# Optimization experiments

Hardware: AMD Instinct MI355X
Metric: run time of the kernel (lower is better)

The kernel has to match this reference:

```python
import jax, jax.numpy as jnp
import numpy as np

B, N, C, G, H, DK = 8, 128, 128, 2, 4, 32
BN_SCALE = float(1.0 / np.sqrt(1.0 + 1e-5))  # eval-mode BatchNorm with running_mean=0, var=1, gamma=1, beta=0


def _l1norm(x):
    # F.normalize(p=1, dim=-1)
    return x / jnp.maximum(jnp.sum(jnp.abs(x), -1, keepdims=True), 1e-12)


def _bn(x):
    return x * BN_SCALE


def _lrelu(x):
    return jax.nn.leaky_relu(x, 0.01)


def setup_inputs() -> dict:
    key = jax.random.key(0)
    ks = jax.random.split(key, 14)
    p = lambda i, shape: jax.random.normal(ks[i], shape, jnp.float32) * 0.05
    return {
        "vp": jax.random.normal(ks[0], (B, N, C), jnp.float32),
        "ep0": jax.random.uniform(ks[1], (B, N, N), jnp.float32),
        # PointSimilarity_Pre 1x1-conv stack (stored as [in, out] matrices)
        "ps_pre_w1": p(2, (C, 2 * C)), "ps_pre_w2": p(3, (2 * C, C)),
        "ps_pre_w3": p(4, (C, 1)), "ps_pre_b3": jnp.zeros((1,), jnp.float32),
        # Per-generation PointSimilarity2 stacks
        "ps_w1": p(5, (G, C, 2 * C)), "ps_w2": p(6, (G, 2 * C, C)),
        "ps_w3": p(7, (G, C, 1)), "ps_b3": jnp.zeros((G, 1), jnp.float32),
        # Per-generation D2PAgg stacks (input is cat(vp, aggr) -> 2C channels)
        "d2p_w1": p(8, (G, 2 * C, 2 * C)), "d2p_w2": p(9, (G, 2 * C, C)),
        # Per-generation multi-head attention projections (d_model=C, n_head*d_k=C)
        "mha_wq": p(10, (G, C, H * DK)), "mha_wk": p(11, (G, C, H * DK)),
    }


def _psim(vp, ep_last, w1, w2, w3, b3, kval):
    # pairwise l2 distance features: [B, N, N, C]
    sim = (vp[:, :, None, :] - vp[:, None, :, :]) ** 2
    h = _lrelu(_bn(jnp.einsum('bijc,co->bijo', sim, w1)))
    h = _lrelu(_bn(jnp.einsum('bijc,co->bijo', h, w2)))
    e = jax.nn.sigmoid(jnp.einsum('bijc,co->bijo', h, w3)[..., 0] + b3)
    eye = jnp.eye(vp.shape[1], dtype=vp.dtype)
    ep_last = ep_last * (1.0 - eye)
    ep_sum = jnp.sum(ep_last, -1, keepdims=True)
    e = e * ep_last
    if kval is not None:  # neighbor attention via top-k sparsification
        _, idx = jax.lax.top_k(e, kval)
        b_i = jnp.arange(e.shape[0])[:, None, None]
        r_i = jnp.arange(e.shape[1])[None, :, None]
        mask = jnp.zeros_like(e).at[b_i, r_i, idx].set(1.0)
        e = e * mask
    e = _l1norm(e) * ep_sum
    e = e + eye + 1e-6
    e = e / jnp.sum(e, 2, keepdims=True)
    return e


def _d2p(ep, vp, w1, w2):
    eye = jnp.eye(vp.shape[1], dtype=vp.dtype)
    edge = _l1norm(ep * (1.0 - eye))
    aggr = jnp.einsum('bij,bjc->bic', edge, vp)  # bmm aggregation
    nf = jnp.concatenate([vp, aggr], -1)         # [B, N, 2C]
    h = _lrelu(_bn(nf @ w1))
    return _lrelu(_bn(h @ w2))


def _mha(vp, wq, wk):
    b, n, _ = vp.shape
    q = (vp @ wq).reshape(b, n, H, DK)
    k = (vp @ wk).reshape(b, n, H, DK)
    attn = jax.nn.softmax(jnp.einsum('bqhd,bkhd->bhqk', q, k) / np.sqrt(DK), axis=-1)
    return attn.mean(1)  # average heads -> [B, N, N]


def reference(vp, ep0, ps_pre_w1, ps_pre_w2, ps_pre_w3, ps_pre_b3,
              ps_w1, ps_w2, ps_w3, ps_b3, d2p_w1, d2p_w2, mha_wq, mha_wk):
    ep = _psim(vp, ep0, ps_pre_w1, ps_pre_w2, ps_pre_w3, ps_pre_b3, None)
    for g in range(G):
        attn = _mha(vp, mha_wq[g], mha_wk[g])
        vp = _d2p(ep * attn, vp, d2p_w1[g], d2p_w2[g])
        kval = int(N * (1.0 - 0.1 * (g + 1)))
        ep = _psim(vp, ep, ps_w1[g], ps_w2[g], ps_w3[g], ps_b3[g], kval)
    return ep
```

## Files before the change

### kernel.cpp

```cpp
#include <hip/hip_runtime.h>

typedef __bf16 bf16x8 __attribute__((ext_vector_type(8)));
typedef float floatx4 __attribute__((ext_vector_type(4)));

#define MFMA(a, b, c) __builtin_amdgcn_mfma_f32_16x16x32_bf16(a, b, c, 0, 0, 0)

#define BNS 0.9999950000374997f
#define LRELU(x) ((x) > 0.f ? (x) : 0.01f * (x))

__device__ inline float wave_sum(float v) {
#pragma unroll
  for (int s = 32; s > 0; s >>= 1) v += __shfl_xor(v, s, 64);
  return v;
}
__device__ inline float wave_max(float v) {
#pragma unroll
  for (int s = 32; s > 0; s >>= 1) v = fmaxf(v, __shfl_xor(v, s, 64));
  return v;
}

__global__ __launch_bounds__(256) void k_prep(const float* __restrict__ pre_w1,
                                              const float* __restrict__ ps_w1,
                                              const float* __restrict__ pre_w2,
                                              const float* __restrict__ ps_w2,
                                              const float* __restrict__ dw1,
                                              const float* __restrict__ dw2,
                                              const float* __restrict__ mwq,
                                              const float* __restrict__ mwk,
                                              __bf16* __restrict__ w1b,
                                              __bf16* __restrict__ w2b,
                                              __bf16* __restrict__ d1i,
                                              __bf16* __restrict__ d2i,
                                              __bf16* __restrict__ qki) {
  const int tt = blockIdx.x * 256 + threadIdx.x;
  bf16x8 v;
  if (tt < 24576) {
    const int buf = tt / 12288;
    const int r = tt % 12288;
    const int set = r >> 12;
    const int q = r & 4095;
    const int ln = q & 63, qd = ln >> 4, cc = ln & 15;
    const int wv = (q >> 6) & 3;
    if (buf == 0) {
      const int kt = (q >> 8) & 3, qtr = (q >> 10) & 3;
      const float* src = (set == 0) ? pre_w1 : ps_w1 + (size_t)(set - 1) * 32768;
      const float* p = src + (size_t)(kt * 32 + qd * 8) * 256 + qtr * 64 + wv * 16 + cc;
#pragma unroll
      for (int jj = 0; jj < 8; jj++) v[jj] = (__bf16)p[jj * 256];
      *(bf16x8*)&w1b[(size_t)set * 32768 + q * 8] = v;
    } else {
      const int kt = (q >> 8) & 1, nt = (q >> 9) & 1, qtr = (q >> 10) & 3;
      const float* src = (set == 0) ? pre_w2 : ps_w2 + (size_t)(set - 1) * 32768;
      const float* p = src + (size_t)(qtr * 64 + kt * 32 + qd * 8) * 128 + wv * 32 + nt * 16 + cc;
#pragma unroll
      for (int jj = 0; jj < 8; jj++) v[jj] = (__bf16)p[jj * 128];
      *(bf16x8*)&w2b[(size_t)set * 32768 + q * 8] = v;
    }
  } else if (tt < 40960) {
    const int u = tt - 24576;
    const int gen = u >> 13, r = u & 8191;
    const int nt = r >> 9, kt = (r >> 6) & 7, ln = r & 63;
    const int qd = ln >> 4, cc = ln & 15;
    const float* src = dw1 + (size_t)gen * 65536 + (size_t)(kt * 32 + qd * 8) * 256 + nt * 16 + cc;
#pragma unroll
    for (int jj = 0; jj < 8; jj++) v[jj] = (__bf16)src[jj * 256];
    *(bf16x8*)&d1i[((size_t)gen * 65536) + (size_t)r * 8] = v;
  } else if (tt < 49152) {
    const int u = tt - 40960;
    const int gen = u >> 12, r = u & 4095;
    const int nt = r >> 9, kt = (r >> 6) & 7, ln = r & 63;
    const int qd = ln >> 4, cc = ln & 15;
    const float* src = dw2 + (size_t)gen * 32768 + (size_t)(kt * 32 + qd * 8) * 128 + nt * 16 + cc;
#pragma unroll
    for (int jj = 0; jj < 8; jj++) v[jj] = (__bf16)src[jj * 128];
    *(bf16x8*)&d2i[((size_t)gen * 32768) + (size_t)r * 8] = v;
  } else if (tt < 57344) {
    const int u = tt - 49152;
    const int gen = u >> 12, r = u & 4095, qk = r >> 11, r2 = r & 2047;
    const int cb = r2 >> 7, o = r2 & 127;
    const float* src = (qk ? mwk : mwq) + (size_t)gen * 16384 + (size_t)(cb * 8) * 128 + o;
#pragma unroll
    for (int jj = 0; jj < 8; jj++) v[jj] = (__bf16)src[jj * 128];
    *(bf16x8*)&qki[(size_t)((((gen * 2 + qk) * 16 + cb) * 128 + o)) * 8] = v;
  }
}

__global__ void __launch_bounds__(256, 3)
k_psim(const float* __restrict__ vp, const float* __restrict__ ep_in,
       float* __restrict__ ep_out,
       const __bf16* __restrict__ w1b, const __bf16* __restrict__ w2b,
       const float* __restrict__ w3, const float* __restrict__ b3,
       int kval, float* __restrict__ outp) {
  __shared__ __bf16 simf[16384];
  __shared__ __bf16 hbf[8192];
  __shared__ float ep_row[128];
  __shared__ float e_row[128];
  __shared__ float w3s[128];
  __shared__ float red[256];
  __shared__ float red2[4];

  const int tid = threadIdx.x;
  const int b = blockIdx.x >> 7, i = blockIdx.x & 127;
  const float* vpb = vp + ((size_t)b << 14);
  const float* vpi = vpb + (i << 7);
  const size_t rowoff = ((size_t)blockIdx.x) << 7;

  const int wv = tid >> 6;
  const int ln = tid & 63;
  const int qd = ln >> 4;
  const int cc = ln & 15;

  {
    const int j = tid >> 1;
    const int c0 = (tid & 1) << 6;
    const int m = j >> 4, ccr = j & 15;
    const float* vpj = vpb + (j << 7) + c0;
    const float* vpx = vpi + c0;
#pragma unroll
    for (int c = 0; c < 64; c += 8) {
      const int gc = c0 + c;
      const int kt = gc >> 5, qdw = (gc >> 3) & 3;
      float4 a0 = *(const float4*)(vpj + c);
      float4 a1 = *(const float4*)(vpj + c + 4);
      float4 b0 = *(const float4*)(vpx + c);
      float4 b1 = *(const float4*)(vpx + c + 4);
      bf16x8 t;
      float d;
      d = a0.x - b0.x; t[0] = (__bf16)(d * d);
      d = a0.y - b0.y; t[1] = (__bf16)(d * d);
      d = a0.z - b0.z; t[2] = (__bf16)(d * d);
      d = a0.w - b0.w; t[3] = (__bf16)(d * d);
      d = a1.x - b1.x; t[4] = (__bf16)(d * d);
      d = a1.y - b1.y; t[5] = (__bf16)(d * d);
      d = a1.z - b1.z; t[6] = (__bf16)(d * d);
      d = a1.w - b1.w; t[7] = (__bf16)(d * d);
      *(bf16x8*)&simf[(((kt << 3) + m) << 6 | (qdw << 4 | ccr)) << 3] = t;
    }
    if (tid < 128) {
      ep_row[tid] = (tid == i) ? 0.f : ep_in[rowoff + tid];
      w3s[tid] = w3[tid];
    }
  }

  bf16x8 bw[4], bw2[2][2];
#pragma unroll
  for (int kt = 0; kt < 4; kt++)
    bw[kt] = *(const bf16x8*)&w1b[(((0 * 4 + kt) * 4 + wv) * 64 + ln) * 8];
#pragma unroll
  for (int nt = 0; nt < 2; nt++)
#pragma unroll
    for (int kt = 0; kt < 2; kt++)
      bw2[nt][kt] = *(const bf16x8*)&w2b[((((0 * 2 + nt) * 2 + kt) * 4 + wv) * 64 + ln) * 8];

  __syncthreads();

  floatx4 acc2[8][2];
#pragma unroll
  for (int m = 0; m < 8; m++) {
    acc2[m][0] = (floatx4){0.f, 0.f, 0.f, 0.f};
    acc2[m][1] = (floatx4){0.f, 0.f, 0.f, 0.f};
  }

  const int h1h = wv >> 1;
  const int h1qd = ((wv & 1) << 1) | (cc >> 3);
  const int h1jj = cc & 7;

#pragma unroll
  for (int qtr = 0; qtr < 4; qtr++) {
    bf16x8 bwn[4], bw2n[2][2];
    if (qtr < 3) {
#pragma unroll
      for (int kt = 0; kt < 4; kt++)
        bwn[kt] = *(const bf16x8*)&w1b[((((qtr + 1) * 4 + kt) * 4 + wv) * 64 + ln) * 8];
#pragma unroll
      for (int nt = 0; nt < 2; nt++)
#pragma unroll
        for (int kt = 0; kt < 2; kt++)
          bw2n[nt][kt] = *(const bf16x8*)&w2b[(((((qtr + 1) * 2 + nt) * 2 + kt) * 4 + wv) * 64 + ln) * 8];
    }

#pragma unroll
    for (int m2 = 0; m2 < 8; m2 += 2) {
      bf16x8 af0[4], af1[4];
#pragma unroll
      for (int kt = 0; kt < 4; kt++) {
        af0[kt] = *(const bf16x8*)&simf[(((kt << 3) + m2) << 6 | ln) << 3];
        af1[kt] = *(const bf16x8*)&simf[(((kt << 3) + m2 + 1) << 6 | ln) << 3];
      }
      floatx4 x0 = (floatx4){0.f, 0.f, 0.f, 0.f};
      floatx4 x1 = (floatx4){0.f, 0.f, 0.f, 0.f};
#pragma unroll
      for (int kt = 0; kt < 4; kt++) {
        x0 = MFMA(af0[kt], bw[kt], x0);
        x1 = MFMA(af1[kt], bw[kt], x1);
      }
#pragma unroll
      for (int r = 0; r < 4; r++) {
        float v0 = x0[r] * BNS;
        float v1 = x1[r] * BNS;
        hbf[(((h1h * 8 + m2) * 64) + h1qd * 16 + qd * 4 + r) * 8 + h1jj] = (__bf16)LRELU(v0);
        hbf[(((h1h * 8 + m2 + 1) * 64) + h1qd * 16 + qd * 4 + r) * 8 + h1jj] = (__bf16)LRELU(v1);
      }
    }
    __syncthreads();

#pragma unroll
    for (int m = 0; m < 8; m++) {
      bf16x8 a0 = *(const bf16x8*)&hbf[((m << 6) | ln) << 3];
      bf16x8 a1 = *(const bf16x8*)&hbf[(((8 + m) << 6) | ln) << 3];
      acc2[m][0] = MFMA(a0, bw2[0][0], acc2[m][0]);
      acc2[m][1] = MFMA(a0, bw2[1][0], acc2[m][1]);
      acc2[m][0] = MFMA(a1, bw2[0][1], acc2[m][0]);
      acc2[m][1] = MFMA(a1, bw2[1][1], acc2[m][1]);
    }
    __syncthreads();

    if (qtr < 3) {
#pragma unroll
      for (int kt = 0; kt < 4; kt++) bw[kt] = bwn[kt];
#pragma unroll
      for (int nt = 0; nt < 2; nt++)
#pragma unroll
        for (int kt = 0; kt < 2; kt++) bw2[nt][kt] = bw2n[nt][kt];
    }
  }

  {
    const int seg = wv;
#pragma unroll
    for (int m = 0; m < 8; m++)
#pragma unroll
      for (int nt = 0; nt < 2; nt++) {
        const int q2 = (nt << 1) | (cc >> 3);
#pragma unroll
        for (int r = 0; r < 4; r++) {
          float v = acc2[m][nt][r] * BNS;
          simf[(((seg * 8 + m) * 64) + q2 * 16 + qd * 4 + r) * 8 + (cc & 7)] = (__bf16)LRELU(v);
        }
      }
  }
  __syncthreads();

  {
    const int j = tid & 127, hh = tid >> 7;
    const int m = j >> 4, R = j & 15;
    float s = 0.f;
#pragma unroll
    for (int sg = 0; sg < 2; sg++) {
      const int seg = hh * 2 + sg;
#pragma unroll
      for (int q3 = 0; q3 < 4; q3++) {
        bf16x8 f = *(const bf16x8*)&simf[(((seg * 8 + m) * 64) + q3 * 16 + R) * 8];
        const float* wp = &w3s[seg * 32 + q3 * 8];
#pragma unroll
        for (int jj = 0; jj < 8; jj++) s += (float)f[jj] * wp[jj];
      }
    }
    red[tid] = s;
  }
  __syncthreads();
  if (tid < 128) {
    float s = red[tid] + red[tid + 128] + b3[0];
    float sg = 1.f / (1.f + expf(-s));
    e_row[tid] = sg * ep_row[tid];
  }
  __syncthreads();

  {
    float v = (tid < 128) ? ep_row[tid] : 0.f;
    float w = wave_sum(v);
    if (ln == 0) red2[wv] = w;
  }
  __syncthreads();
  const float ep_sum = red2[0] + red2[1];

  if (kval > 0) {
    const int j = tid & 127, hh = tid >> 7;
    const float v = e_row[j];
    int cnt = 0;
    const int base = hh << 6;
#pragma unroll 8
    for (int jj = 0; jj < 64; jj++) {
      float u = e_row[base + jj];
      cnt += (u > v || (u == v && (base + jj) < j)) ? 1 : 0;
    }
    red[tid] = (float)cnt;
  }
  __syncthreads();

  float em = 0.f;
  if (tid < 128) {
    float v = e_row[tid];
    if (kval > 0) {
      int cnt = (int)red[tid] + (int)red[tid + 128];
      em = (cnt < kval) ? v : 0.f;
    } else {
      em = v;
    }
  }
  {
    float w = wave_sum((tid < 128) ? em : 0.f);
    if (ln == 0) red2[wv] = w;
  }
  __syncthreads();
  const float l1 = red2[0] + red2[1];
  __syncthreads();

  const float scale = ep_sum / fmaxf(l1, 1e-12f);
  float val = 0.f;
  if (tid < 128) val = em * scale + ((tid == i) ? 1.f : 0.f) + 1e-6f;
  {
    float w = wave_sum((tid < 128) ? val : 0.f);
    if (ln == 0) red2[wv] = w;
  }
  __syncthreads();
  const float rsum = red2[0] + red2[1];

  if (tid < 128) {
    float o = val / rsum;
    ep_out[rowoff + tid] = o;
    if (outp) outp[rowoff + tid] = o;
  }
}

__global__ __launch_bounds__(256) void k_qk(const float* __restrict__ vp,
                                            const __bf16* __restrict__ qkw,
                                            float* __restrict__ qo,
                                            float* __restrict__ ko) {
  __shared__ float vr[128];
  const int t = threadIdx.x;
  const size_t rowoff = ((size_t)blockIdx.x) << 7;
  if (t < 128) vr[t] = vp[rowoff + t];
  __syncthreads();
  const int o = t & 127;
  const __bf16* base = qkw + ((t >> 7) ? 16384 : 0);
  const float4* vr4 = (const float4*)vr;
  float a = 0.f;
#pragma unroll
  for (int cb = 0; cb < 16; cb++) {
    bf16x8 w8 = *(const bf16x8*)&base[(cb * 128 + o) * 8];
    float4 v0 = vr4[2 * cb], v1 = vr4[2 * cb + 1];
    a += v0.x * (float)w8[0] + v0.y * (float)w8[1] + v0.z * (float)w8[2] + v0.w * (float)w8[3] +
         v1.x * (float)w8[4] + v1.y * (float)w8[5] + v1.z * (float)w8[6] + v1.w * (float)w8[7];
  }
  float* dst = (t < 128) ? qo : ko;
  dst[rowoff + o] = a;
}

__global__ __launch_bounds__(256) void k_attn_agg(const float* __restrict__ qv,
                                                  const float* __restrict__ kv,
                                                  const float* __restrict__ ep,
                                                  const float* __restrict__ vp_in,
                                                  float* __restrict__ agg) {
  __shared__ float qi[256];
  __shared__ float sbuf[1024];
  __shared__ float er[256];
  __shared__ float pbuf[2048];
  __shared__ float red2[4];

  const int tid = threadIdx.x;
  const int wv = tid >> 6, ln = tid & 63;
  const int b = blockIdx.x >> 6;
  const int r0 = (blockIdx.x & 63) * 2;
  const size_t rowoff0 = ((size_t)(b * 128 + r0)) << 7;
  const float* vpbb = vp_in + ((size_t)b << 14);

  qi[tid] = qv[rowoff0 + tid];
  __syncthreads();

  {
    const int j = tid & 127, hh = tid >> 7;
    const float* krow = kv + (((size_t)(b * 128 + j)) << 7);
    const int h0 = hh * 2, h1 = hh * 2 + 1;
    float s00 = 0.f, s01 = 0.f, s10 = 0.f, s11 = 0.f;
#pragma unroll
    for (int d = 0; d < 32; d += 4) {
      float4 k0 = *(const float4*)(krow + h0 * 32 + d);
      float4 k1 = *(const float4*)(krow + h1 * 32 + d);
      s00 += qi[h0 * 32 + d] * k0.x + qi[h0 * 32 + d + 1] * k0.y +
             qi[h0 * 32 + d + 2] * k0.z + qi[h0 * 32 + d + 3] * k0.w;
      s01 += qi[h1 * 32 + d] * k1.x + qi[h1 * 32 + d + 1] * k1.y +
             qi[h1 * 32 + d + 2] * k1.z + qi[h1 * 32 + d + 3] * k1.w;
      s10 += qi[128 + h0 * 32 + d] * k0.x + qi[128 + h0 * 32 + d + 1] * k0.y +
             qi[128 + h0 * 32 + d + 2] * k0.z + qi[128 + h0 * 32 + d + 3] * k0.w;
      s11 += qi[128 + h1 * 32 + d] * k1.x + qi[128 + h1 * 32 + d + 1] * k1.y +
             qi[128 + h1 * 32 + d + 2] * k1.z + qi[128 + h1 * 32 + d + 3] * k1.w;
    }
    const float sc = 0.17677669529663687f;
    sbuf[(0 * 4 + h0) * 128 + j] = s00 * sc;
    sbuf[(0 * 4 + h1) * 128 + j] = s01 * sc;
    sbuf[(1 * 4 + h0) * 128 + j] = s10 * sc;
    sbuf[(1 * 4 + h1) * 128 + j] = s11 * sc;
  }
  __syncthreads();

  {
    const int g = wv;
#pragma unroll
    for (int row = 0; row < 2; row++) {
      float a = sbuf[(row * 4 + g) * 128 + ln];
      float bb = sbuf[(row * 4 + g) * 128 + 64 + ln];
      float mx = wave_max(fmaxf(a, bb));
      float e0 = expf(a - mx), e1 = expf(bb - mx);
      float Z = wave_sum(e0 + e1);
      sbuf[(row * 4 + g) * 128 + ln] = e0 / Z;
      sbuf[(row * 4 + g) * 128 + 64 + ln] = e1 / Z;
    }
  }
  __syncthreads();

  {
    const int row = tid >> 7, j = tid & 127;
    float attn = 0.25f * (sbuf[(row * 4) * 128 + j] + sbuf[(row * 4 + 1) * 128 + j] +
                          sbuf[(row * 4 + 2) * 128 + j] + sbuf[(row * 4 + 3) * 128 + j]);
    float eraw = (j == r0 + row) ? 0.f : ep[rowoff0 + tid] * attn;
    float w = wave_sum(eraw);
    if (ln == 0) red2[wv] = w;
    __syncthreads();
    float l1row = red2[row * 2] + red2[row * 2 + 1];
    er[tid] = eraw / fmaxf(l1row, 1e-12f);
  }
  __syncthreads();

  {
    const int cg = tid & 31, jg = tid >> 5;
    float4 a0 = {0.f, 0.f, 0.f, 0.f}, a1 = {0.f, 0.f, 0.f, 0.f};
#pragma unroll
    for (int jj = 0; jj < 16; jj++) {
      const int j = jg * 16 + jj;
      float4 v = *(const float4*)(vpbb + (j << 7) + (cg << 2));
      float e0 = er[j], e1 = er[128 + j];
      a0.x += e0 * v.x; a0.y += e0 * v.y; a0.z += e0 * v.z; a0.w += e0 * v.w;
      a1.x += e1 * v.x; a1.y += e1 * v.y; a1.z += e1 * v.z; a1.w += e1 * v.w;
    }
    *(float4*)&pbuf[(jg * 32 + cg) * 4] = a0;
    *(float4*)&pbuf[1024 + (jg * 32 + cg) * 4] = a1;
  }
  __syncthreads();
  {
    const int row = tid >> 7, c = tid & 127;
    float s = 0.f;
#pragma unroll
    for (int jg = 0; jg < 8; jg++) s += pbuf[(row << 10) + jg * 128 + c];
    agg[rowoff0 + tid] = s;
  }
}

__global__ __launch_bounds__(256) void k_mlp(const float* __restrict__ vp_in,
                                             const float* __restrict__ agg,
                                             const __bf16* __restrict__ d1,
                                             const __bf16* __restrict__ d2,
                                             float* __restrict__ vp_out) {
  __shared__ __bf16 hls[4096];
  const int tid = threadIdx.x;
  const int wv = tid >> 6, ln = tid & 63, qd = ln >> 4, cc = ln & 15;
  const int row = (blockIdx.x << 4) + cc;

  bf16x8 af[8];
#pragma unroll
  for (int kt = 0; kt < 4; kt++) {
    const float* p = vp_in + (size_t)row * 128 + kt * 32 + qd * 8;
    float4 v0 = *(const float4*)p, v1 = *(const float4*)(p + 4);
    bf16x8 t;
    t[0] = (__bf16)v0.x; t[1] = (__bf16)v0.y; t[2] = (__bf16)v0.z; t[3] = (__bf16)v0.w;
    t[4] = (__bf16)v1.x; t[5] = (__bf16)v1.y; t[6] = (__bf16)v1.z; t[7] = (__bf16)v1.w;
    af[kt] = t;
  }
#pragma unroll
  for (int kt = 0; kt < 4; kt++) {
    const float* p = agg + (size_t)row * 128 + kt * 32 + qd * 8;
    float4 v0 = *(const float4*)p, v1 = *(const float4*)(p + 4);
    bf16x8 t;
    t[0] = (__bf16)v0.x; t[1] = (__bf16)v0.y; t[2] = (__bf16)v0.z; t[3] = (__bf16)v0.w;
    t[4] = (__bf16)v1.x; t[5] = (__bf16)v1.y; t[6] = (__bf16)v1.z; t[7] = (__bf16)v1.w;
    af[4 + kt] = t;
  }

#pragma unroll
  for (int nt = 0; nt < 4; nt++) {
    const int ntg = wv * 4 + nt;
    floatx4 acc = (floatx4){0.f, 0.f, 0.f, 0.f};
#pragma unroll
    for (int kt = 0; kt < 8; kt++) {
      bf16x8 bw = *(const bf16x8*)&d1[((size_t)(ntg * 8 + kt) * 64 + ln) * 8];
      acc = MFMA(af[kt], bw, acc);
    }
    const int col = ntg * 16 + cc;
    const int kt2 = col >> 5, qd2 = (col >> 3) & 3, jjs = col & 7;
#pragma unroll
    for (int r = 0; r < 4; r++) {
      float h = acc[r] * BNS;
      const int m = qd * 4 + r;
      hls[((kt2 * 64) + qd2 * 16 + m) * 8 + jjs] = (__bf16)LRELU(h);
    }
  }
  __syncthreads();

  bf16x8 a2[8];
#pragma unroll
  for (int kt2 = 0; kt2 < 8; kt2++)
    a2[kt2] = *(const bf16x8*)&hls[(kt2 * 64 + ln) * 8];
#pragma unroll
  for (int nt = 0; nt < 2; nt++) {
    const int ntg = wv * 2 + nt;
    floatx4 o = (floatx4){0.f, 0.f, 0.f, 0.f};
#pragma unroll
    for (int kt2 = 0; kt2 < 8; kt2++) {
      bf16x8 bw = *(const bf16x8*)&d2[((size_t)(ntg * 8 + kt2) * 64 + ln) * 8];
      o = MFMA(a2[kt2], bw, o);
    }
    const int col = ntg * 16 + cc;
#pragma unroll
    for (int r = 0; r < 4; r++) {
      float v = o[r] * BNS;
      const int m = qd * 4 + r;
      vp_out[(size_t)((blockIdx.x << 4) + m) * 128 + col] = LRELU(v);
    }
  }
}

extern "C" void kernel_launch(void* const* d_in, const int* in_sizes, int n_in,
                              void* d_out, int out_size, void* d_ws, size_t ws_size,
                              hipStream_t stream) {
  const float* vp0    = (const float*)d_in[0];
  const float* ep0    = (const float*)d_in[1];
  const float* pre_w1 = (const float*)d_in[2];
  const float* pre_w2 = (const float*)d_in[3];
  const float* pre_w3 = (const float*)d_in[4];
  const float* pre_b3 = (const float*)d_in[5];
  const float* ps_w1  = (const float*)d_in[6];
  const float* ps_w2  = (const float*)d_in[7];
  const float* ps_w3  = (const float*)d_in[8];
  const float* ps_b3  = (const float*)d_in[9];
  const float* dw1    = (const float*)d_in[10];
  const float* dw2    = (const float*)d_in[11];
  const float* mwq    = (const float*)d_in[12];
  const float* mwk    = (const float*)d_in[13];

  char* ws = (char*)d_ws;
  float* ep   = (float*)(ws);
  float* vpb  = (float*)(ws + (512ull << 10));
  float* vpa  = (float*)(ws + (1024ull << 10));
  float* qf   = (float*)(ws + (1536ull << 10));
  float* kf   = (float*)(ws + (2048ull << 10));
  __bf16* w1b = (__bf16*)(ws + (2560ull << 10));
  __bf16* w2b = (__bf16*)(ws + (2560ull << 10) + 196608);
  __bf16* d1i = (__bf16*)(ws + (2560ull << 10) + 393216);
  __bf16* d2i = (__bf16*)(ws + (2560ull << 10) + 655360);
  __bf16* qki = (__bf16*)(ws + (2560ull << 10) + 786432);
  float* agg  = (float*)(ws + (2560ull << 10) + 917504);
  float* outp = (float*)d_out;

  k_prep<<<224, 256, 0, stream>>>(pre_w1, ps_w1, pre_w2, ps_w2, dw1, dw2, mwq, mwk,
                                  w1b, w2b, d1i, d2i, qki);

  k_psim<<<1024, 256, 0, stream>>>(vp0, ep0, ep, w1b, w2b, pre_w3, pre_b3, 0, nullptr);

  k_qk<<<1024, 256, 0, stream>>>(vp0, qki, qf, kf);
  k_attn_agg<<<512, 256, 0, stream>>>(qf, kf, ep, vp0, agg);
  k_mlp<<<64, 256, 0, stream>>>(vp0, agg, d1i, d2i, vpb);
  k_psim<<<1024, 256, 0, stream>>>(vpb, ep, ep, w1b + 32768, w2b + 32768,
                                   ps_w3, ps_b3, 115, nullptr);

  k_qk<<<1024, 256, 0, stream>>>(vpb, qki + 32768, qf, kf);
  k_attn_agg<<<512, 256, 0, stream>>>(qf, kf, ep, vpb, agg);
  k_mlp<<<64, 256, 0, stream>>>(vpb, agg, d1i + 65536, d2i + 32768, vpa);
  k_psim<<<1024, 256, 0, stream>>>(vpa, ep, ep, w1b + 65536, w2b + 65536,
                                   ps_w3 + 128, ps_b3 + 1, 102, outp);
}
```

Before: 222.4 us.

## Shrink psim LDS footprint and register pressure to fit four blocks per CU

Raises the psim kernel's occupancy target from 3 to 4 blocks per CU. It halves the hidden-layer LDS buffer by splitting each quarter's row tiles into two halves with an extra barrier pair, and aliases the small scratch arrays onto that buffer. It also drops the prefetch of next-quarter weights and keeps the ep row in a register to reduce VGPR pressure. The trade is more synchronisation and exposed global weight-load latency in exchange for more resident waves to hide latency.

```diff
diff --git a/kernel.cpp b/kernel.cpp
--- a/kernel.cpp
+++ b/kernel.cpp
@@ -85,19 +85,19 @@
   }
 }
 
-__global__ void __launch_bounds__(256, 3)
+__global__ void __launch_bounds__(256, 4)
 k_psim(const float* __restrict__ vp, const float* __restrict__ ep_in,
        float* __restrict__ ep_out,
        const __bf16* __restrict__ w1b, const __bf16* __restrict__ w2b,
        const float* __restrict__ w3, const float* __restrict__ b3,
        int kval, float* __restrict__ outp) {
   __shared__ __bf16 simf[16384];
-  __shared__ __bf16 hbf[8192];
-  __shared__ float ep_row[128];
-  __shared__ float e_row[128];
-  __shared__ float w3s[128];
-  __shared__ float red[256];
-  __shared__ float red2[4];
+  __shared__ __align__(16) char sc2[8192];
+  __bf16* hbf   = (__bf16*)sc2;
+  float* red    = (float*)sc2;
+  float* e_row  = (float*)(sc2 + 1024);
+  float* red2   = (float*)(sc2 + 1536);
+  float* w3s    = (float*)(sc2 + 1552);
 
   const int tid = threadIdx.x;
   const int b = blockIdx.x >> 7, i = blockIdx.x & 127;
@@ -110,6 +110,7 @@
   const int qd = ln >> 4;
   const int cc = ln & 15;
 
+  float ep_reg = 0.f;
   {
     const int j = tid >> 1;
     const int c0 = (tid & 1) << 6;
@@ -136,22 +137,8 @@
       d = a1.w - b1.w; t[7] = (__bf16)(d * d);
       *(bf16x8*)&simf[(((kt << 3) + m) << 6 | (qdw << 4 | ccr)) << 3] = t;
     }
-    if (tid < 128) {
-      ep_row[tid] = (tid == i) ? 0.f : ep_in[rowoff + tid];
-      w3s[tid] = w3[tid];
-    }
-  }
-
-  bf16x8 bw[4], bw2[2][2];
-#pragma unroll
-  for (int kt = 0; kt < 4; kt++)
-    bw[kt] = *(const bf16x8*)&w1b[(((0 * 4 + kt) * 4 + wv) * 64 + ln) * 8];
-#pragma unroll
-  for (int nt = 0; nt < 2; nt++)
-#pragma unroll
-    for (int kt = 0; kt < 2; kt++)
-      bw2[nt][kt] = *(const bf16x8*)&w2b[((((0 * 2 + nt) * 2 + kt) * 4 + wv) * 64 + ln) * 8];
-
+    if (tid < 128) ep_reg = (tid == i) ? 0.f : ep_in[rowoff + tid];
+  }
   __syncthreads();
 
   floatx4 acc2[8][2];
@@ -165,63 +152,55 @@
   const int h1qd = ((wv & 1) << 1) | (cc >> 3);
   const int h1jj = cc & 7;
 
-#pragma unroll
   for (int qtr = 0; qtr < 4; qtr++) {
-    bf16x8 bwn[4], bw2n[2][2];
-    if (qtr < 3) {
-#pragma unroll
-      for (int kt = 0; kt < 4; kt++)
-        bwn[kt] = *(const bf16x8*)&w1b[((((qtr + 1) * 4 + kt) * 4 + wv) * 64 + ln) * 8];
-#pragma unroll
-      for (int nt = 0; nt < 2; nt++)
-#pragma unroll
-        for (int kt = 0; kt < 2; kt++)
-          bw2n[nt][kt] = *(const bf16x8*)&w2b[(((((qtr + 1) * 2 + nt) * 2 + kt) * 4 + wv) * 64 + ln) * 8];
-    }
-
-#pragma unroll
-    for (int m2 = 0; m2 < 8; m2 += 2) {
-      bf16x8 af0[4], af1[4];
-#pragma unroll
-      for (int kt = 0; kt < 4; kt++) {
-        af0[kt] = *(const bf16x8*)&simf[(((kt << 3) + m2) << 6 | ln) << 3];
-        af1[kt] = *(const bf16x8*)&simf[(((kt << 3) + m2 + 1) << 6 | ln) << 3];
+    bf16x8 bw[4], bw2[2][2];
+#pragma unroll
+    for (int kt = 0; kt < 4; kt++)
+      bw[kt] = *(const bf16x8*)&w1b[((((qtr * 4 + kt) * 4 + wv) * 64) + ln) * 8];
+#pragma unroll
+    for (int nt = 0; nt < 2; nt++)
+#pragma unroll
+      for (int kt = 0; kt < 2; kt++)
+        bw2[nt][kt] = *(const bf16x8*)&w2b[(((((qtr * 2 + nt) * 2 + kt) * 4 + wv) * 64) + ln) * 8];
+
+    for (int mh = 0; mh < 2; mh++) {
+#pragma unroll
+      for (int m2p = 0; m2p < 4; m2p += 2) {
+        const int m2 = 4 * mh + m2p;
+        bf16x8 af0[4], af1[4];
+#pragma unroll
+        for (int kt = 0; kt < 4; kt++) {
+          af0[kt] = *(const bf16x8*)&simf[(((kt << 3) + m2) << 6 | ln) << 3];
+          af1[kt] = *(const bf16x8*)&simf[(((kt << 3) + m2 + 1) << 6 | ln) << 3];
+        }
+        floatx4 x0 = (floatx4){0.f, 0.f, 0.f, 0.f};
+        floatx4 x1 = (floatx4){0.f, 0.f, 0.f, 0.f};
+#pragma unroll
+        for (int kt = 0; kt < 4; kt++) {
+          x0 = MFMA(af0[kt], bw[kt], x0);
+          x1 = MFMA(af1[kt], bw[kt], x1);
+        }
+#pragma unroll
+        for (int r = 0; r < 4; r++) {
+          float v0 = x0[r] * BNS;
+          float v1 = x1[r] * BNS;
+          hbf[(((h1h * 4 + m2p) * 64) + h1qd * 16 + qd * 4 + r) * 8 + h1jj] = (__bf16)LRELU(v0);
+          hbf[(((h1h * 4 + m2p + 1) * 64) + h1qd * 16 + qd * 4 + r) * 8 + h1jj] = (__bf16)LRELU(v1);
+        }
       }
-      floatx4 x0 = (floatx4){0.f, 0.f, 0.f, 0.f};
-      floatx4 x1 = (floatx4){0.f, 0.f, 0.f, 0.f};
-#pragma unroll
-      for (int kt = 0; kt < 4; kt++) {
-        x0 = MFMA(af0[kt], bw[kt], x0);
-        x1 = MFMA(af1[kt], bw[kt], x1);
+      __syncthreads();
+
+#pragma unroll
+      for (int ml = 0; ml < 4; ml++) {
+        bf16x8 a0 = *(const bf16x8*)&hbf[((0 * 4 + ml) * 64 + ln) * 8];
+        bf16x8 a1 = *(const bf16x8*)&hbf[((1 * 4 + ml) * 64 + ln) * 8];
+        const int m = 4 * mh + ml;
+        acc2[m][0] = MFMA(a0, bw2[0][0], acc2[m][0]);
+        acc2[m][1] = MFMA(a0, bw2[1][0], acc2[m][1]);
+        acc2[m][0] = MFMA(a1, bw2[0][1], acc2[m][0]);
+        acc2[m][1] = MFMA(a1, bw2[1][1], acc2[m][1]);
       }
-#pragma unroll
-      for (int r = 0; r < 4; r++) {
-        float v0 = x0[r] * BNS;
-        float v1 = x1[r] * BNS;
-        hbf[(((h1h * 8 + m2) * 64) + h1qd * 16 + qd * 4 + r) * 8 + h1jj] = (__bf16)LRELU(v0);
-        hbf[(((h1h * 8 + m2 + 1) * 64) + h1qd * 16 + qd * 4 + r) * 8 + h1jj] = (__bf16)LRELU(v1);
-      }
-    }
-    __syncthreads();
-
-#pragma unroll
-    for (int m = 0; m < 8; m++) {
-      bf16x8 a0 = *(const bf16x8*)&hbf[((m << 6) | ln) << 3];
-      bf16x8 a1 = *(const bf16x8*)&hbf[(((8 + m) << 6) | ln) << 3];
-      acc2[m][0] = MFMA(a0, bw2[0][0], acc2[m][0]);
-      acc2[m][1] = MFMA(a0, bw2[1][0], acc2[m][1]);
-      acc2[m][0] = MFMA(a1, bw2[0][1], acc2[m][0]);
-      acc2[m][1] = MFMA(a1, bw2[1][1], acc2[m][1]);
-    }
-    __syncthreads();
-
-    if (qtr < 3) {
-#pragma unroll
-      for (int kt = 0; kt < 4; kt++) bw[kt] = bwn[kt];
-#pragma unroll
-      for (int nt = 0; nt < 2; nt++)
-#pragma unroll
-        for (int kt = 0; kt < 2; kt++) bw2[nt][kt] = bw2n[nt][kt];
+      __syncthreads();
     }
   }
 
@@ -238,6 +217,7 @@
           simf[(((seg * 8 + m) * 64) + q2 * 16 + qd * 4 + r) * 8 + (cc & 7)] = (__bf16)LRELU(v);
         }
       }
+    if (tid < 128) w3s[tid] = w3[tid];
   }
   __syncthreads();
 
@@ -262,12 +242,12 @@
   if (tid < 128) {
     float s = red[tid] + red[tid + 128] + b3[0];
     float sg = 1.f / (1.f + expf(-s));
-    e_row[tid] = sg * ep_row[tid];
-  }
-  __syncthreads();
-
-  {
-    float v = (tid < 128) ? ep_row[tid] : 0.f;
+    e_row[tid] = sg * ep_reg;
+  }
+  __syncthreads();
+
+  {
+    float v = (tid < 128) ? ep_reg : 0.f;
     float w = wave_sum(v);
     if (ln == 0) red2[wv] = w;
   }
```

Measured after the change: 235.1 us. 5.7% more time.
